# Kernel optimization log

Hardware: AMD Instinct MI355X
Metric: run time of the kernel (lower is better)

The kernel has to match this reference:

```python
import jax, jax.numpy as jnp
import numpy as np

B, D_INNER, D_STATE, DT_RANK = 512, 5120, 16, 160


def setup_inputs() -> dict:
    key = jax.random.key(0)
    ks = jax.random.split(key, 9)
    s = lambda fan: 1.0 / np.sqrt(fan)
    x = jax.random.normal(ks[0], (B, 1, 1, D_INNER), dtype=jnp.float32)
    W_dt_rank = jax.random.normal(ks[1], (DT_RANK, D_INNER), dtype=jnp.float32) * s(D_INNER)
    W_dt = jax.random.normal(ks[2], (D_INNER, DT_RANK), dtype=jnp.float32) * s(DT_RANK)
    b_dt = jax.random.normal(ks[3], (D_INNER,), dtype=jnp.float32)
    W_B = jax.random.normal(ks[4], (D_STATE, D_INNER), dtype=jnp.float32) * s(D_INNER)
    W_C = jax.random.normal(ks[5], (D_STATE, D_INNER), dtype=jnp.float32) * s(D_INNER)
    # A = -exp(A_log) as in preprocess_A; keep entries negative
    A = -jnp.exp(jax.random.normal(ks[6], (D_INNER, D_STATE), dtype=jnp.float32) * 0.5)
    D = jax.random.normal(ks[7], (D_INNER,), dtype=jnp.float32)
    h = jax.random.normal(ks[8], (B, D_INNER, D_STATE), dtype=jnp.float32) * 0.1
    return {"x": x, "W_dt_rank": W_dt_rank, "W_dt": W_dt, "b_dt": b_dt,
            "W_B": W_B, "W_C": W_C, "A": A, "D": D, "h": h}


def reference(x, W_dt_rank, W_dt, b_dt, W_B, W_C, A, D, h):
    # x: [B,1,1,d_inner] -> [B,d_inner]
    xf = x.reshape(B, D_INNER)
    # delta_t: low-rank dt projection + dt_proj + softplus -> [B,d_inner]
    dt = jax.nn.softplus(jnp.einsum('br,dr->bd', jnp.einsum('bd,rd->br', xf, W_dt_rank), W_dt) + b_dt)
    Bc = jnp.einsum('bd,sd->bs', xf, W_B)  # [B,d_state]
    Cc = jnp.einsum('bd,sd->bs', xf, W_C)  # [B,d_state]
    # delta_A = exp(A * dt), broadcast dt over d_state  -> [B,d_inner,d_state]
    dA = jnp.exp(A[None, :, :] * dt[:, :, None])
    # delta_B = dt * B, broadcast B over d_inner -> [B,d_inner,d_state]
    dB = dt[:, :, None] * Bc[:, None, :]
    # hidden state update
    h_new = dA * h + dB * xf[:, :, None]
    # y = h_new @ C + D * x  -> [B,d_inner]
    y = jnp.einsum('bds,bs->bd', h_new, Cc) + D[None, :] * xf
    return y.reshape(B, 1, 1, D_INNER)
```

## Files before the change

### kernel.cpp

```cpp
#include <hip/hip_runtime.h>
#include <math.h>

#define BATCH 512
#define DIN   5120
#define DST   16
#define RK    160
#define NJ    192
#define NZ1   16

typedef __attribute__((ext_vector_type(8))) __bf16 bf16x8;
typedef __attribute__((ext_vector_type(4))) float f32x4;
typedef __attribute__((ext_vector_type(8))) unsigned short ushort8;

#define OFF_XP    0u
#define OFF_WP    5242880u
#define OFF_WDTP  7208960u
#define OFF_PART  8847360u
#define OFF_DTRP  15138816u
#define OFF_B     15302656u
#define OFF_C     15335424u

__device__ __forceinline__ unsigned short f2bf(float f) {
  unsigned int u = __float_as_uint(f);
  u = (u + 0x7FFFu + ((u >> 16) & 1u)) >> 16;
  return (unsigned short)u;
}

#define N1 (512*640)
#define N2 (192*640)
__global__ __launch_bounds__(256) void k_prep(
    const float* __restrict__ x, const float* __restrict__ Wdtr,
    const float* __restrict__ WB, const float* __restrict__ WC,
    const float* __restrict__ Wdt, char* __restrict__ ws)
{
  const int tid = blockIdx.x * 256 + threadIdx.x;
  const float* src; unsigned long long dst_idx;
  if (tid < N1) {
    const int b = tid / 640, k8 = tid - b * 640;
    src = x + (size_t)b * DIN + k8 * 8;
    dst_idx = (OFF_XP >> 4) + (size_t)k8 * 512 + b;
  } else if (tid < N1 + N2) {
    const int i = tid - N1;
    const int j = i / 640, k8 = i - j * 640;
    const float* row;
    if (j < RK)            row = Wdtr + (size_t)j * DIN;
    else if (j < RK + DST) row = WB   + (size_t)(j - RK) * DIN;
    else                   row = WC   + (size_t)(j - RK - DST) * DIN;
    src = row + k8 * 8;
    dst_idx = (OFF_WP >> 4) + (size_t)k8 * 192 + j;
  } else {
    const int i = tid - N1 - N2;
    const int d = i / 20, k8 = i - d * 20;
    src = Wdt + (size_t)d * RK + k8 * 8;
    dst_idx = (OFF_WDTP >> 4) + (size_t)k8 * 5120 + d;
  }
  const float4 f0 = *(const float4*)(src);
  const float4 f1 = *(const float4*)(src + 4);
  ushort8 o;
  o[0]=f2bf(f0.x); o[1]=f2bf(f0.y); o[2]=f2bf(f0.z); o[3]=f2bf(f0.w);
  o[4]=f2bf(f1.x); o[5]=f2bf(f1.y); o[6]=f2bf(f1.z); o[7]=f2bf(f1.w);
  ((ushort8*)ws)[dst_idx] = o;
}

__global__ __launch_bounds__(256) void k_g1(char* __restrict__ ws)
{
  const int wid  = blockIdx.x * 4 + (threadIdx.x >> 6);
  const int l    = threadIdx.x & 63;
  const int z    = wid / 384;
  const int rem  = wid - z * 384;
  const int jt   = rem >> 5;
  const int bt   = rem & 31;
  const int j0   = jt * 16, b0 = bt * 16;

  const bf16x8* WPv = (const bf16x8*)(ws + OFF_WP);
  const bf16x8* xPv = (const bf16x8*)(ws + OFF_XP);
  float* part = (float*)(ws + OFF_PART);

  const int lg = l >> 4, lr = l & 15;
  f32x4 acc = {0.f, 0.f, 0.f, 0.f};

#pragma unroll 2
  for (int s = 0; s < 10; ++s) {
    const int k8 = z * 40 + s * 4 + lg;
    const bf16x8 av = WPv[(size_t)k8 * 192 + j0 + lr];
    const bf16x8 bv = xPv[(size_t)k8 * 512 + b0 + lr];
    acc = __builtin_amdgcn_mfma_f32_16x16x32_bf16(av, bv, acc, 0, 0, 0);
  }

  float* pb = part + (size_t)wid * 256;
#pragma unroll
  for (int r = 0; r < 4; ++r)
    pb[(lg * 4 + r) * 16 + lr] = acc[r];
}

__global__ __launch_bounds__(256) void k_red1(char* __restrict__ ws)
{
  const int e = blockIdx.x * 256 + threadIdx.x;
  const int j = e >> 9, b = e & 511;
  const int jt = j >> 4, jr = j & 15, bt = b >> 4, bc = b & 15;

  const float* part = (const float*)(ws + OFF_PART);
  float s = 0.f;
#pragma unroll
  for (int z = 0; z < NZ1; ++z)
    s += part[((size_t)(z * 384 + jt * 32 + bt) << 8) + jr * 16 + bc];

  if (j < RK) {
    unsigned short* dtrP = (unsigned short*)(ws + OFF_DTRP);
    dtrP[((size_t)(j >> 3) * 512 + b) * 8 + (j & 7)] = f2bf(s);
  } else if (j < RK + DST) {
    ((float*)(ws + OFF_B))[(size_t)b * DST + (j - RK)] = s;
  } else {
    ((float*)(ws + OFF_C))[(size_t)b * DST + (j - RK - DST)] = s;
  }
}

__global__ __launch_bounds__(256) void k_g2y(
    const float* __restrict__ bdt, const float* __restrict__ A,
    const float* __restrict__ Dp,  const float* __restrict__ x,
    const float* __restrict__ h,   float* __restrict__ y,
    char* __restrict__ ws)
{
  __shared__ float sDT[4][16][17];
  __shared__ float sB[4][16][16];
  __shared__ float sC[4][16][16];
  __shared__ float sX[4][16][16];

  const int w = threadIdx.x >> 6;
  const int l = threadIdx.x & 63;
  const int wid = blockIdx.x * 4 + w;
  const int dtile = wid % 320, btile = wid / 320;
  const int d0 = dtile * 16, b0 = btile * 16;

  const bf16x8* dtrPv = (const bf16x8*)(ws + OFF_DTRP);
  const bf16x8* WdtPv = (const bf16x8*)(ws + OFF_WDTP);
  const float*  Bc    = (const float*)(ws + OFF_B);
  const float*  Cc    = (const float*)(ws + OFF_C);

  *(float4*)&((float*)sB[w])[l * 4] = *(const float4*)&Bc[b0 * DST + l * 4];
  *(float4*)&((float*)sC[w])[l * 4] = *(const float4*)&Cc[b0 * DST + l * 4];
  {
    const int xr = l >> 2, xc = (l & 3) * 4;
    *(float4*)&sX[w][xr][xc] = *(const float4*)&x[(size_t)(b0 + xr) * DIN + d0 + xc];
  }

  const int lg = l >> 4, lr = l & 15;
  f32x4 acc = {0.f, 0.f, 0.f, 0.f};
#pragma unroll
  for (int s = 0; s < 5; ++s) {
    const int k8 = s * 4 + lg;
    const bf16x8 av = dtrPv[(size_t)k8 * 512 + b0 + lr];
    const bf16x8 bv = WdtPv[(size_t)k8 * 5120 + d0 + lr];
    acc = __builtin_amdgcn_mfma_f32_16x16x32_bf16(av, bv, acc, 0, 0, 0);
  }
  const float bias = bdt[d0 + lr];
#pragma unroll
  for (int r = 0; r < 4; ++r) {
    const float pre = acc[r] + bias;
    sDT[w][lg * 4 + r][lr] = (pre > 20.f) ? pre : log1pf(__expf(pre));
  }
  __syncthreads();

  const int q = l & 3;
  const int Q = l >> 2;
  const int d = d0 + Q;
  const float4 A4 = *(const float4*)(A + (size_t)d * DST + q * 4);
  const float  Dv = Dp[d];

  const float* hp = h + ((size_t)b0 * DIN + d) * DST + q * 4;
  float* yp = y + (size_t)b0 * DIN + d;

  float4 hbuf[4];
#pragma unroll
  for (int j = 0; j < 4; ++j)
    hbuf[j] = *(const float4*)(hp + (size_t)j * (DIN * DST));

#pragma unroll
  for (int j = 0; j < 16; ++j) {
    const float4 h4 = hbuf[j & 3];
    if (j + 4 < 16)
      hbuf[j & 3] = *(const float4*)(hp + (size_t)(j + 4) * (DIN * DST));

    const float dtv = sDT[w][j][Q];
    const float xv  = sX[w][j][Q];
    const float dtx = dtv * xv;
    const float4 B4 = *(const float4*)&sB[w][j][q * 4];
    const float4 C4 = *(const float4*)&sC[w][j][q * 4];

    const float dA0 = __expf(A4.x * dtv);
    const float dA1 = __expf(A4.y * dtv);
    const float dA2 = __expf(A4.z * dtv);
    const float dA3 = __expf(A4.w * dtv);
    const float hn0 = fmaf(dA0, h4.x, dtx * B4.x);
    const float hn1 = fmaf(dA1, h4.y, dtx * B4.y);
    const float hn2 = fmaf(dA2, h4.z, dtx * B4.z);
    const float hn3 = fmaf(dA3, h4.w, dtx * B4.w);
    float p = hn0 * C4.x + hn1 * C4.y + hn2 * C4.z + hn3 * C4.w;

    p += __shfl_xor(p, 1);
    p += __shfl_xor(p, 2);
    if (q == 0) yp[(size_t)j * DIN] = fmaf(Dv, xv, p);
  }
}

extern "C" void kernel_launch(void* const* d_in, const int* in_sizes, int n_in,
                              void* d_out, int out_size, void* d_ws, size_t ws_size,
                              hipStream_t stream) {
  const float* x    = (const float*)d_in[0];
  const float* Wdtr = (const float*)d_in[1];
  const float* Wdt  = (const float*)d_in[2];
  const float* bdt  = (const float*)d_in[3];
  const float* WB   = (const float*)d_in[4];
  const float* WC   = (const float*)d_in[5];
  const float* A    = (const float*)d_in[6];
  const float* Dp   = (const float*)d_in[7];
  const float* h    = (const float*)d_in[8];
  float* y = (float*)d_out;
  char* ws = (char*)d_ws;

  k_prep<<<dim3(2160), 256, 0, stream>>>(x, Wdtr, WB, WC, Wdt, ws);
  k_g1<<<dim3(1536), 256, 0, stream>>>(ws);
  k_red1<<<dim3(384), 256, 0, stream>>>(ws);
  k_g2y<<<dim3(2560), 256, 0, stream>>>(bdt, A, Dp, x, h, y, ws);
}
```

Before: 56.63 us.

## Replace split-K GEMM plus reduction kernel with direct full-K per-wave GEMM

The first projection GEMM no longer splits K into 16 chunks that write partial tiles and then get summed in a separate reduction kernel. Each of 384 single-wave blocks now walks the full K range with four independent MFMA accumulators and writes dtr/B/C directly. This removes one kernel launch and the partial-sum round trip through global memory. In exchange it launches far fewer waves (384 on a 256-CU device), so parallelism and latency hiding in this stage drop.

```diff
diff --git a/kernel.cpp b/kernel.cpp
--- a/kernel.cpp
+++ b/kernel.cpp
@@ -6,7 +6,6 @@
 #define DST   16
 #define RK    160
 #define NJ    192
-#define NZ1   16
 
 typedef __attribute__((ext_vector_type(8))) __bf16 bf16x8;
 typedef __attribute__((ext_vector_type(4))) float f32x4;
@@ -15,7 +14,6 @@
 #define OFF_XP    0u
 #define OFF_WP    5242880u
 #define OFF_WDTP  7208960u
-#define OFF_PART  8847360u
 #define OFF_DTRP  15138816u
 #define OFF_B     15302656u
 #define OFF_C     15335424u
@@ -62,56 +60,54 @@
   ((ushort8*)ws)[dst_idx] = o;
 }
 
-__global__ __launch_bounds__(256) void k_g1(char* __restrict__ ws)
+__global__ __launch_bounds__(64) void k_g1d(char* __restrict__ ws)
 {
-  const int wid  = blockIdx.x * 4 + (threadIdx.x >> 6);
-  const int l    = threadIdx.x & 63;
-  const int z    = wid / 384;
-  const int rem  = wid - z * 384;
-  const int jt   = rem >> 5;
-  const int bt   = rem & 31;
-  const int j0   = jt * 16, b0 = bt * 16;
+  const int wid = blockIdx.x;
+  const int l   = threadIdx.x;
+  const int jt  = wid >> 5, bt = wid & 31;
+  const int j0  = jt * 16, b0 = bt * 16;
 
   const bf16x8* WPv = (const bf16x8*)(ws + OFF_WP);
   const bf16x8* xPv = (const bf16x8*)(ws + OFF_XP);
-  float* part = (float*)(ws + OFF_PART);
 
   const int lg = l >> 4, lr = l & 15;
-  f32x4 acc = {0.f, 0.f, 0.f, 0.f};
-
-#pragma unroll 2
-  for (int s = 0; s < 10; ++s) {
-    const int k8 = z * 40 + s * 4 + lg;
-    const bf16x8 av = WPv[(size_t)k8 * 192 + j0 + lr];
-    const bf16x8 bv = xPv[(size_t)k8 * 512 + b0 + lr];
-    acc = __builtin_amdgcn_mfma_f32_16x16x32_bf16(av, bv, acc, 0, 0, 0);
-  }
-
-  float* pb = part + (size_t)wid * 256;
-#pragma unroll
-  for (int r = 0; r < 4; ++r)
-    pb[(lg * 4 + r) * 16 + lr] = acc[r];
-}
-
-__global__ __launch_bounds__(256) void k_red1(char* __restrict__ ws)
-{
-  const int e = blockIdx.x * 256 + threadIdx.x;
-  const int j = e >> 9, b = e & 511;
-  const int jt = j >> 4, jr = j & 15, bt = b >> 4, bc = b & 15;
-
-  const float* part = (const float*)(ws + OFF_PART);
-  float s = 0.f;
-#pragma unroll
-  for (int z = 0; z < NZ1; ++z)
-    s += part[((size_t)(z * 384 + jt * 32 + bt) << 8) + jr * 16 + bc];
-
-  if (j < RK) {
+  f32x4 a0 = {0.f,0.f,0.f,0.f}, a1 = a0, a2 = a0, a3 = a0;
+
+  for (int s = 0; s < 40; ++s) {
+    const int base = s * 16 + lg;
+    a0 = __builtin_amdgcn_mfma_f32_16x16x32_bf16(
+        WPv[(size_t)(base +  0) * 192 + j0 + lr],
+        xPv[(size_t)(base +  0) * 512 + b0 + lr], a0, 0, 0, 0);
+    a1 = __builtin_amdgcn_mfma_f32_16x16x32_bf16(
+        WPv[(size_t)(base +  4) * 192 + j0 + lr],
+        xPv[(size_t)(base +  4) * 512 + b0 + lr], a1, 0, 0, 0);
+    a2 = __builtin_amdgcn_mfma_f32_16x16x32_bf16(
+        WPv[(size_t)(base +  8) * 192 + j0 + lr],
+        xPv[(size_t)(base +  8) * 512 + b0 + lr], a2, 0, 0, 0);
+    a3 = __builtin_amdgcn_mfma_f32_16x16x32_bf16(
+        WPv[(size_t)(base + 12) * 192 + j0 + lr],
+        xPv[(size_t)(base + 12) * 512 + b0 + lr], a3, 0, 0, 0);
+  }
+  const f32x4 acc = (a0 + a1) + (a2 + a3);
+
+  const int b = b0 + lr;
+  if (jt < 10) {
     unsigned short* dtrP = (unsigned short*)(ws + OFF_DTRP);
-    dtrP[((size_t)(j >> 3) * 512 + b) * 8 + (j & 7)] = f2bf(s);
-  } else if (j < RK + DST) {
-    ((float*)(ws + OFF_B))[(size_t)b * DST + (j - RK)] = s;
+#pragma unroll
+    for (int r = 0; r < 4; ++r) {
+      const int j = j0 + lg * 4 + r;
+      dtrP[((size_t)(j >> 3) * 512 + b) * 8 + (j & 7)] = f2bf(acc[r]);
+    }
+  } else if (jt == 10) {
+    float* Bc = (float*)(ws + OFF_B);
+#pragma unroll
+    for (int r = 0; r < 4; ++r)
+      Bc[(size_t)b * DST + lg * 4 + r] = acc[r];
   } else {
-    ((float*)(ws + OFF_C))[(size_t)b * DST + (j - RK - DST)] = s;
+    float* Cc = (float*)(ws + OFF_C);
+#pragma unroll
+    for (int r = 0; r < 4; ++r)
+      Cc[(size_t)b * DST + lg * 4 + r] = acc[r];
   }
 }
 
@@ -219,7 +215,6 @@
   char* ws = (char*)d_ws;
 
   k_prep<<<dim3(2160), 256, 0, stream>>>(x, Wdtr, WB, WC, Wdt, ws);
-  k_g1<<<dim3(1536), 256, 0, stream>>>(ws);
-  k_red1<<<dim3(384), 256, 0, stream>>>(ws);
+  k_g1d<<<dim3(384), 64, 0, stream>>>(ws);
   k_g2y<<<dim3(2560), 256, 0, stream>>>(bdt, A, Dp, x, h, y, ws);
 }
```

Result: slower. 97.68 us (+72.5%).
